# Kernel tuning notes

Measured on AMD Instinct MI355X. Metric: run time of the kernel, lower is better.

Reference implementation:

```python
import jax, jax.numpy as jnp
import numpy as np
import math

NH = 8   # num heads
DH = 64  # d_head = 512/8
D = 512
L = 6

def _pe(seq, d):
    pos = np.arange(seq, dtype=np.float32)[:, None]
    div = np.exp(np.arange(0, d, 2, dtype=np.float32) * (-math.log(10000.0) / d))
    pe = np.zeros((seq, d), dtype=np.float32)
    pe[:, 0::2] = np.sin(pos * div)
    pe[:, 1::2] = np.cos(pos * div)
    return jnp.asarray(pe)

def _ln(x, g, b, eps=1e-6):
    m = x.mean(-1, keepdims=True)
    v = ((x - m) ** 2).mean(-1, keepdims=True)  # unbiased=False
    return g * (x - m) / jnp.sqrt(v + eps) + b

def _mha(q_in, k_in, v_in, qkv_w, qkv_b, o_w, o_b, mask):
    b, sq, d = q_in.shape
    sk = k_in.shape[1]
    q = (q_in @ qkv_w[0] + qkv_b[0]).reshape(b, sq, NH, DH).transpose(0, 2, 1, 3)  # [b,h,sq,dh]
    k = (k_in @ qkv_w[1] + qkv_b[1]).reshape(b, sk, NH, DH).transpose(0, 2, 1, 3)
    v = (v_in @ qkv_w[2] + qkv_b[2]).reshape(b, sk, NH, DH).transpose(0, 2, 1, 3)
    scores = jnp.einsum('bhqd,bhkd->bhqk', q, k) / math.sqrt(DH)  # [b,h,sq,sk]
    if mask is not None:
        scores = jnp.where(mask, -jnp.inf, scores)  # mask True = masked, broadcast over b,h
    w = jax.nn.softmax(scores, axis=-1)
    out = jnp.einsum('bhqk,bhkd->bhqd', w, v).transpose(0, 2, 1, 3).reshape(b, sq, d)
    return out @ o_w + o_b

def _ff(x, w1, b1, w2, b2):
    return jax.nn.relu(x @ w1 + b1) @ w2 + b2

def reference(src, tgt, src_emb, tgt_emb,
              enc_qkv_w, enc_qkv_b, enc_o_w, enc_o_b,
              enc_ff_w1, enc_ff_b1, enc_ff_w2, enc_ff_b2,
              enc_ln_g, enc_ln_b, enc_fg, enc_fb,
              dec_sqkv_w, dec_sqkv_b, dec_so_w, dec_so_b,
              dec_cqkv_w, dec_cqkv_b, dec_co_w, dec_co_b,
              dec_ff_w1, dec_ff_b1, dec_ff_w2, dec_ff_b2,
              dec_ln_g, dec_ln_b, dec_fg, dec_fb):
    S, T = src.shape[1], tgt.shape[1]
    scale = math.sqrt(D)
    # ---- encoder (pre-LN) ----
    x = src_emb[src] * scale + _pe(S, D)  # [b,S,d]
    for i in range(L):
        h = _ln(x, enc_ln_g[i, 0], enc_ln_b[i, 0])
        x = x + _mha(h, h, h, enc_qkv_w[i], enc_qkv_b[i], enc_o_w[i], enc_o_b[i], None)
        h = _ln(x, enc_ln_g[i, 1], enc_ln_b[i, 1])
        x = x + _ff(h, enc_ff_w1[i], enc_ff_b1[i], enc_ff_w2[i], enc_ff_b2[i])
    memory = _ln(x, enc_fg, enc_fb)
    # ---- decoder (pre-LN) ----
    causal = jnp.triu(jnp.ones((T, T), dtype=bool), 1)  # True above diagonal = masked
    y = tgt_emb[tgt] * scale + _pe(T, D)  # [b,T,d]
    for i in range(L):
        h = _ln(y, dec_ln_g[i, 0], dec_ln_b[i, 0])
        y = y + _mha(h, h, h, dec_sqkv_w[i], dec_sqkv_b[i], dec_so_w[i], dec_so_b[i], causal)
        h = _ln(y, dec_ln_g[i, 1], dec_ln_b[i, 1])
        y = y + _mha(h, memory, memory, dec_cqkv_w[i], dec_cqkv_b[i], dec_co_w[i], dec_co_b[i], None)
        h = _ln(y, dec_ln_g[i, 2], dec_ln_b[i, 2])
        y = y + _ff(h, dec_ff_w1[i], dec_ff_b1[i], dec_ff_w2[i], dec_ff_b2[i])
    return _ln(y, dec_fg, dec_fb)

def setup_inputs():
    key = jax.random.key(0)
    ks = iter(jax.random.split(key, 40))
    B, S, T, V, DFF = 8, 128, 128, 32000, 2048
    s = 0.02
    inp = {
        'src': jax.random.randint(next(ks), (B, S), 0, V, dtype=jnp.int32),
        'tgt': jax.random.randint(next(ks), (B, T), 0, V, dtype=jnp.int32),
        'src_emb': jax.random.normal(next(ks), (V, D), jnp.float32) * s,
        'tgt_emb': jax.random.normal(next(ks), (V, D), jnp.float32) * s,
        'enc_qkv_w': jax.random.normal(next(ks), (L, 3, D, D), jnp.float32) * s,
        'enc_qkv_b': jnp.zeros((L, 3, D), jnp.float32),
        'enc_o_w': jax.random.normal(next(ks), (L, D, D), jnp.float32) * s,
        'enc_o_b': jnp.zeros((L, D), jnp.float32),
        'enc_ff_w1': jax.random.normal(next(ks), (L, D, DFF), jnp.float32) * s,
        'enc_ff_b1': jnp.zeros((L, DFF), jnp.float32),
        'enc_ff_w2': jax.random.normal(next(ks), (L, DFF, D), jnp.float32) * s,
        'enc_ff_b2': jnp.zeros((L, D), jnp.float32),
        'enc_ln_g': jnp.ones((L, 2, D), jnp.float32),
        'enc_ln_b': jnp.zeros((L, 2, D), jnp.float32),
        'enc_fg': jnp.ones((D,), jnp.float32),
        'enc_fb': jnp.zeros((D,), jnp.float32),
        'dec_sqkv_w': jax.random.normal(next(ks), (L, 3, D, D), jnp.float32) * s,
        'dec_sqkv_b': jnp.zeros((L, 3, D), jnp.float32),
        'dec_so_w': jax.random.normal(next(ks), (L, D, D), jnp.float32) * s,
        'dec_so_b': jnp.zeros((L, D), jnp.float32),
        'dec_cqkv_w': jax.random.normal(next(ks), (L, 3, D, D), jnp.float32) * s,
        'dec_cqkv_b': jnp.zeros((L, 3, D), jnp.float32),
        'dec_co_w': jax.random.normal(next(ks), (L, D, D), jnp.float32) * s,
        'dec_co_b': jnp.zeros((L, D), jnp.float32),
        'dec_ff_w1': jax.random.normal(next(ks), (L, D, DFF), jnp.float32) * s,
        'dec_ff_b1': jnp.zeros((L, DFF), jnp.float32),
        'dec_ff_w2': jax.random.normal(next(ks), (L, DFF, D), jnp.float32) * s,
        'dec_ff_b2': jnp.zeros((L, D), jnp.float32),
        'dec_ln_g': jnp.ones((L, 3, D), jnp.float32),
        'dec_ln_b': jnp.zeros((L, 3, D), jnp.float32),
        'dec_fg': jnp.ones((D,), jnp.float32),
        'dec_fb': jnp.zeros((D,), jnp.float32),
    }
    return inp
```

## Files before the change

kernel.cpp:

```cpp
#include <hip/hip_runtime.h>
#include <hip/hip_bf16.h>
#include <math.h>

#define D 512
#define NH 8
#define DHEAD 64
#define LAYERS 6
#define DFF 2048
#define BATCH 8
#define SEQ 128
#define ROWS (BATCH * SEQ)

typedef float f32x4 __attribute__((ext_vector_type(4)));
typedef short bf16x8 __attribute__((ext_vector_type(8)));

__device__ __forceinline__ unsigned short f2b(float x) {
    return __builtin_bit_cast(unsigned short, __float2bfloat16(x));
}

__global__ __launch_bounds__(256) void embed_pe_kernel(const int* __restrict__ tok,
        const float* __restrict__ emb, float* __restrict__ out)
{
    int i = blockIdx.x * 256 + threadIdx.x;
    int bs = i >> 9;
    int d  = i & 511;
    int s  = bs & (SEQ - 1);
    int tk = tok[bs];
    float dv  = expf(-(float)(d & ~1) * (9.210340371976184f / 512.0f));
    float arg = (float)s * dv;
    float pe  = (d & 1) ? cosf(arg) : sinf(arg);
    out[i] = emb[(size_t)tk * D + d] * 22.627416997969522f + pe;
}

__global__ __launch_bounds__(256) void transpose_cvt_kernel(
        const float* __restrict__ in, unsigned short* __restrict__ out, int R, int C)
{
    __shared__ float t[32][33];
    const size_t moff = (size_t)blockIdx.z * R * C;
    const float* src = in + moff;
    unsigned short* dst = out + moff;
    const int r0 = blockIdx.y << 5, c0 = blockIdx.x << 5;
    const int tid = threadIdx.x;
    const int rr = tid >> 3, cc = (tid & 7) << 2;
    float4 v = *(const float4*)(src + (size_t)(r0 + rr) * C + c0 + cc);
    t[rr][cc] = v.x; t[rr][cc + 1] = v.y; t[rr][cc + 2] = v.z; t[rr][cc + 3] = v.w;
    __syncthreads();
    const int oc = tid >> 3, or4 = (tid & 7) << 2;
    ushort4 o;
    o.x = f2b(t[or4 + 0][oc]);
    o.y = f2b(t[or4 + 1][oc]);
    o.z = f2b(t[or4 + 2][oc]);
    o.w = f2b(t[or4 + 3][oc]);
    *(ushort4*)(dst + (size_t)(c0 + oc) * R + r0 + or4) = o;
}

template<int OUT_BF16>
__global__ __launch_bounds__(256) void ln_kernel(const float* __restrict__ x,
        const float* __restrict__ g, const float* __restrict__ bta,
        void* __restrict__ outp)
{
    int lane = threadIdx.x & 63;
    int row  = (blockIdx.x << 2) + (threadIdx.x >> 6);
    const float* xr = x + (size_t)row * D;
    int c = lane * 8;
    float4 v0 = *(const float4*)(xr + c);
    float4 v1 = *(const float4*)(xr + c + 4);
    float s  = v0.x + v0.y + v0.z + v0.w + v1.x + v1.y + v1.z + v1.w;
    float sq = v0.x*v0.x + v0.y*v0.y + v0.z*v0.z + v0.w*v0.w
             + v1.x*v1.x + v1.y*v1.y + v1.z*v1.z + v1.w*v1.w;
    #pragma unroll
    for (int o = 32; o; o >>= 1) {
        s  += __shfl_xor(s, o);
        sq += __shfl_xor(sq, o);
    }
    float mean = s * (1.0f / D);
    float var  = sq * (1.0f / D) - mean * mean;
    float inv  = rsqrtf(var + 1e-6f);
    float4 g0 = *(const float4*)(g + c),   g1 = *(const float4*)(g + c + 4);
    float4 b0 = *(const float4*)(bta + c), b1 = *(const float4*)(bta + c + 4);
    float4 o0, o1;
    o0.x = g0.x * (v0.x - mean) * inv + b0.x;
    o0.y = g0.y * (v0.y - mean) * inv + b0.y;
    o0.z = g0.z * (v0.z - mean) * inv + b0.z;
    o0.w = g0.w * (v0.w - mean) * inv + b0.w;
    o1.x = g1.x * (v1.x - mean) * inv + b1.x;
    o1.y = g1.y * (v1.y - mean) * inv + b1.y;
    o1.z = g1.z * (v1.z - mean) * inv + b1.z;
    o1.w = g1.w * (v1.w - mean) * inv + b1.w;
    if (OUT_BF16) {
        unsigned short* orow = (unsigned short*)outp + (size_t)row * D + c;
        uint4 o;
        o.x = (unsigned int)f2b(o0.x) | ((unsigned int)f2b(o0.y) << 16);
        o.y = (unsigned int)f2b(o0.z) | ((unsigned int)f2b(o0.w) << 16);
        o.z = (unsigned int)f2b(o1.x) | ((unsigned int)f2b(o1.y) << 16);
        o.w = (unsigned int)f2b(o1.z) | ((unsigned int)f2b(o1.w) << 16);
        *(uint4*)orow = o;
    } else {
        float* orow = (float*)outp + (size_t)row * D + c;
        *(float4*)(orow)     = o0;
        *(float4*)(orow + 4) = o1;
    }
}

template<int RESID, int RELU, int OUT_BF16>
__global__ __launch_bounds__(256) void mgemm_kernel(
        const unsigned short* __restrict__ A,
        const unsigned short* __restrict__ Wt,
        const float* __restrict__ bias,
        const float* __restrict__ Rp,
        void* __restrict__ Cout,
        int N, int K,
        long aZ, long wZ, long bZ, long cZ)
{
    __shared__ unsigned short As[2][64][72];
    __shared__ unsigned short Bs[2][64][72];
    const long z = blockIdx.z;
    const unsigned short* Ab = A  + z * aZ;
    const unsigned short* Wb = Wt + z * wZ;
    const float* biasb = bias + z * bZ;
    const int tid  = threadIdx.x;
    const int lane = tid & 63, wid = tid >> 6;
    const int wm = wid >> 1, wn = wid & 1;
    const int bm = blockIdx.y << 6, bn = blockIdx.x << 6;
    const int srow = tid >> 2, sk = (tid & 3) << 4;
    const unsigned short* Ag = Ab + (size_t)(bm + srow) * K + sk;
    const unsigned short* Bg = Wb + (size_t)(bn + srow) * K + sk;
    const int fr = lane & 15;
    const int fk = (lane >> 4) << 3;
    f32x4 acc[2][2];
    #pragma unroll
    for (int i = 0; i < 2; ++i)
        #pragma unroll
        for (int j = 0; j < 2; ++j)
            acc[i][j] = (f32x4){0.f, 0.f, 0.f, 0.f};

    uint4 a0 = *(const uint4*)Ag, a1 = *(const uint4*)(Ag + 8);
    uint4 b0 = *(const uint4*)Bg, b1 = *(const uint4*)(Bg + 8);
    const int T = K >> 6;
    for (int t = 0; t < T; ++t) {
        const int p = t & 1;
        *(uint4*)&As[p][srow][sk]     = a0;
        *(uint4*)&As[p][srow][sk + 8] = a1;
        *(uint4*)&Bs[p][srow][sk]     = b0;
        *(uint4*)&Bs[p][srow][sk + 8] = b1;
        if (t + 1 < T) {
            Ag += 64; Bg += 64;
            a0 = *(const uint4*)Ag; a1 = *(const uint4*)(Ag + 8);
            b0 = *(const uint4*)Bg; b1 = *(const uint4*)(Bg + 8);
        }
        __syncthreads();
        #pragma unroll
        for (int s = 0; s < 2; ++s) {
            bf16x8 af0 = *(const bf16x8*)&As[p][wm * 32 + fr][s * 32 + fk];
            bf16x8 af1 = *(const bf16x8*)&As[p][wm * 32 + 16 + fr][s * 32 + fk];
            bf16x8 bf0 = *(const bf16x8*)&Bs[p][wn * 32 + fr][s * 32 + fk];
            bf16x8 bf1 = *(const bf16x8*)&Bs[p][wn * 32 + 16 + fr][s * 32 + fk];
            acc[0][0] = __builtin_amdgcn_mfma_f32_16x16x32_bf16(af0, bf0, acc[0][0], 0, 0, 0);
            acc[0][1] = __builtin_amdgcn_mfma_f32_16x16x32_bf16(af0, bf1, acc[0][1], 0, 0, 0);
            acc[1][0] = __builtin_amdgcn_mfma_f32_16x16x32_bf16(af1, bf0, acc[1][0], 0, 0, 0);
            acc[1][1] = __builtin_amdgcn_mfma_f32_16x16x32_bf16(af1, bf1, acc[1][1], 0, 0, 0);
        }
    }
    const int cr   = (lane >> 4) << 2;
    const int ccol = lane & 15;
    #pragma unroll
    for (int i = 0; i < 2; ++i)
        #pragma unroll
        for (int j = 0; j < 2; ++j) {
            int col = bn + wn * 32 + j * 16 + ccol;
            float bsv = biasb[col];
            #pragma unroll
            for (int r = 0; r < 4; ++r) {
                int row = bm + wm * 32 + i * 16 + cr + r;
                float v = acc[i][j][r] + bsv;
                if (RESID) v += Rp[(size_t)row * N + col];
                if (RELU)  v = fmaxf(v, 0.f);
                if (OUT_BF16) ((unsigned short*)Cout + z * cZ)[(size_t)row * N + col] = f2b(v);
                else          ((float*)Cout)[(size_t)row * N + col] = v;
            }
        }
}

template<int CAUSAL>
__global__ __launch_bounds__(256) void attn_kernel(
        const unsigned short* __restrict__ Qp, int qs,
        const unsigned short* __restrict__ Kp,
        const unsigned short* __restrict__ Vp, int kvs,
        unsigned short* __restrict__ Op, int os)
{
    __shared__ unsigned short Ks[128 * 72];
    __shared__ unsigned short Qs[64 * 72];
    __shared__ unsigned short Vt[64 * 136];
    __shared__ unsigned short Ps[64 * 136];
    const int bh    = blockIdx.x >> 1;
    const int qbase = (blockIdx.x & 1) << 6;
    const int brow  = (bh >> 3) * SEQ;
    const int hoff  = (bh & 7) * DHEAD;
    const int tid = threadIdx.x, lane = tid & 63, wid = tid >> 6;

    #pragma unroll
    for (int it = 0; it < 4; ++it) {
        int idx = it * 256 + tid;
        int row = idx >> 3;
        int c8  = (idx & 7) << 3;
        *(uint4*)&Ks[row * 72 + c8] =
            *(const uint4*)(Kp + (size_t)(brow + row) * kvs + hoff + c8);
        uint4 vu = *(const uint4*)(Vp + (size_t)(brow + row) * kvs + hoff + c8);
        unsigned arr[4] = {vu.x, vu.y, vu.z, vu.w};
        #pragma unroll
        for (int j = 0; j < 8; ++j)
            Vt[(c8 + j) * 136 + row] = (unsigned short)(arr[j >> 1] >> ((j & 1) * 16));
    }
    #pragma unroll
    for (int it = 0; it < 2; ++it) {
        int idx = it * 256 + tid;
        int row = idx >> 3;
        int c8  = (idx & 7) << 3;
        *(uint4*)&Qs[row * 72 + c8] =
            *(const uint4*)(Qp + (size_t)(brow + qbase + row) * qs + hoff + c8);
    }
    __syncthreads();

    const int fr = lane & 15, fg = lane >> 4;
    f32x4 accs[8];
    #pragma unroll
    for (int kf = 0; kf < 8; ++kf) accs[kf] = (f32x4){0.f, 0.f, 0.f, 0.f};
    bf16x8 aq0 = *(const bf16x8*)&Qs[(wid * 16 + fr) * 72 + fg * 8];
    bf16x8 aq1 = *(const bf16x8*)&Qs[(wid * 16 + fr) * 72 + 32 + fg * 8];
    #pragma unroll
    for (int kf = 0; kf < 8; ++kf) {
        bf16x8 bk0 = *(const bf16x8*)&Ks[(kf * 16 + fr) * 72 + fg * 8];
        bf16x8 bk1 = *(const bf16x8*)&Ks[(kf * 16 + fr) * 72 + 32 + fg * 8];
        accs[kf] = __builtin_amdgcn_mfma_f32_16x16x32_bf16(aq0, bk0, accs[kf], 0, 0, 0);
        accs[kf] = __builtin_amdgcn_mfma_f32_16x16x32_bf16(aq1, bk1, accs[kf], 0, 0, 0);
    }
    const float SC = 0.125f * 1.44269504f;
    float linv[4];
    #pragma unroll
    for (int r = 0; r < 4; ++r) {
        int qrow = qbase + wid * 16 + fg * 4 + r;
        float sv[8];
        #pragma unroll
        for (int kf = 0; kf < 8; ++kf) {
            float s = accs[kf][r] * SC;
            if (CAUSAL) {
                int key = kf * 16 + fr;
                if (key > qrow) s = -1e30f;
            }
            sv[kf] = s;
        }
        float m = sv[0];
        #pragma unroll
        for (int kf = 1; kf < 8; ++kf) m = fmaxf(m, sv[kf]);
        #pragma unroll
        for (int o = 1; o < 16; o <<= 1) m = fmaxf(m, __shfl_xor(m, o));
        float l = 0.f;
        #pragma unroll
        for (int kf = 0; kf < 8; ++kf) {
            float p = exp2f(sv[kf] - m);
            l += p;
            Ps[(wid * 16 + fg * 4 + r) * 136 + kf * 16 + fr] = f2b(p);
        }
        #pragma unroll
        for (int o = 1; o < 16; o <<= 1) l += __shfl_xor(l, o);
        linv[r] = 1.f / l;
    }
    f32x4 acco[4];
    #pragma unroll
    for (int df = 0; df < 4; ++df) acco[df] = (f32x4){0.f, 0.f, 0.f, 0.f};
    #pragma unroll
    for (int ks = 0; ks < 4; ++ks) {
        bf16x8 pa = *(const bf16x8*)&Ps[(wid * 16 + fr) * 136 + ks * 32 + fg * 8];
        #pragma unroll
        for (int df = 0; df < 4; ++df) {
            bf16x8 vb = *(const bf16x8*)&Vt[(df * 16 + fr) * 136 + ks * 32 + fg * 8];
            acco[df] = __builtin_amdgcn_mfma_f32_16x16x32_bf16(pa, vb, acco[df], 0, 0, 0);
        }
    }
    #pragma unroll
    for (int df = 0; df < 4; ++df)
        #pragma unroll
        for (int r = 0; r < 4; ++r) {
            int qrow = qbase + wid * 16 + fg * 4 + r;
            Op[(size_t)(brow + qrow) * os + hoff + df * 16 + fr] = f2b(acco[df][r] * linv[r]);
        }
}

extern "C" void kernel_launch(void* const* d_in, const int* in_sizes, int n_in,
                              void* d_out, int out_size, void* d_ws, size_t ws_size,
                              hipStream_t stream)
{
    const int*   src       = (const int*)d_in[0];
    const int*   tgt       = (const int*)d_in[1];
    const float* src_emb   = (const float*)d_in[2];
    const float* tgt_emb   = (const float*)d_in[3];
    const float* enc_qkv_w = (const float*)d_in[4];
    const float* enc_qkv_b = (const float*)d_in[5];
    const float* enc_o_w   = (const float*)d_in[6];
    const float* enc_o_b   = (const float*)d_in[7];
    const float* enc_ff_w1 = (const float*)d_in[8];
    const float* enc_ff_b1 = (const float*)d_in[9];
    const float* enc_ff_w2 = (const float*)d_in[10];
    const float* enc_ff_b2 = (const float*)d_in[11];
    const float* enc_ln_g  = (const float*)d_in[12];
    const float* enc_ln_b  = (const float*)d_in[13];
    const float* enc_fg    = (const float*)d_in[14];
    const float* enc_fb    = (const float*)d_in[15];
    const float* dec_sqkv_w = (const float*)d_in[16];
    const float* dec_sqkv_b = (const float*)d_in[17];
    const float* dec_so_w   = (const float*)d_in[18];
    const float* dec_so_b   = (const float*)d_in[19];
    const float* dec_cqkv_w = (const float*)d_in[20];
    const float* dec_cqkv_b = (const float*)d_in[21];
    const float* dec_co_w   = (const float*)d_in[22];
    const float* dec_co_b   = (const float*)d_in[23];
    const float* dec_ff_w1  = (const float*)d_in[24];
    const float* dec_ff_b1  = (const float*)d_in[25];
    const float* dec_ff_w2  = (const float*)d_in[26];
    const float* dec_ff_b2  = (const float*)d_in[27];
    const float* dec_ln_g   = (const float*)d_in[28];
    const float* dec_ln_b   = (const float*)d_in[29];
    const float* dec_fg     = (const float*)d_in[30];
    const float* dec_fb     = (const float*)d_in[31];

    unsigned short* wp = (unsigned short*)d_ws;
    unsigned short* WencQKV  = wp; wp += (size_t)6 * 786432;
    unsigned short* WencO    = wp; wp += (size_t)6 * 262144;
    unsigned short* WencF1   = wp; wp += (size_t)6 * 1048576;
    unsigned short* WencF2   = wp; wp += (size_t)6 * 1048576;
    unsigned short* WdecSQKV = wp; wp += (size_t)6 * 786432;
    unsigned short* WdecSO   = wp; wp += (size_t)6 * 262144;
    unsigned short* WdecCQKV = wp; wp += (size_t)6 * 786432;
    unsigned short* WdecCO   = wp; wp += (size_t)6 * 262144;
    unsigned short* WdecF1   = wp; wp += (size_t)6 * 1048576;
    unsigned short* WdecF2   = wp; wp += (size_t)6 * 1048576;
    unsigned short* Hb   = wp; wp += ROWS * D;
    unsigned short* QKVb = wp; wp += ROWS * 3 * D;
    unsigned short* CQb  = wp; wp += ROWS * D;
    unsigned short* CKVall = wp; wp += (size_t)6 * ROWS * 1024;
    unsigned short* ATTb = wp; wp += ROWS * D;
    unsigned short* F1b  = wp; wp += ROWS * DFF;
    unsigned short* MEMb = wp; wp += ROWS * D;
    float* X = (float*)wp;

    auto T = [&](const float* in, unsigned short* out, int R_, int C_, int n) {
        transpose_cvt_kernel<<<dim3(C_ / 32, R_ / 32, n), 256, 0, stream>>>(in, out, R_, C_);
    };
    T(enc_qkv_w,  WencQKV,  512, 512, 18);
    T(enc_o_w,    WencO,    512, 512, 6);
    T(enc_ff_w1,  WencF1,   512, DFF, 6);
    T(enc_ff_w2,  WencF2,   DFF, 512, 6);
    T(dec_sqkv_w, WdecSQKV, 512, 512, 18);
    T(dec_so_w,   WdecSO,   512, 512, 6);
    T(dec_cqkv_w, WdecCQKV, 512, 512, 18);
    T(dec_co_w,   WdecCO,   512, 512, 6);
    T(dec_ff_w1,  WdecF1,   512, DFF, 6);
    T(dec_ff_w2,  WdecF2,   DFF, 512, 6);

    embed_pe_kernel<<<2048, 256, 0, stream>>>(src, src_emb, X);
    for (int i = 0; i < LAYERS; ++i) {
        ln_kernel<1><<<256, 256, 0, stream>>>(X, enc_ln_g + (size_t)(i*2+0)*D, enc_ln_b + (size_t)(i*2+0)*D, Hb);
        mgemm_kernel<0,0,1><<<dim3(24,16,1), 256, 0, stream>>>(Hb, WencQKV + (size_t)i*786432,
                enc_qkv_b + (size_t)i*1536, nullptr, QKVb, 1536, 512, 0, 0, 0, 0);
        attn_kernel<0><<<128, 256, 0, stream>>>(QKVb, 1536, QKVb + 512, QKVb + 1024, 1536, ATTb, 512);
        mgemm_kernel<1,0,0><<<dim3(8,16,1), 256, 0, stream>>>(ATTb, WencO + (size_t)i*262144,
                enc_o_b + (size_t)i*512, X, X, 512, 512, 0, 0, 0, 0);
        ln_kernel<1><<<256, 256, 0, stream>>>(X, enc_ln_g + (size_t)(i*2+1)*D, enc_ln_b + (size_t)(i*2+1)*D, Hb);
        mgemm_kernel<0,1,1><<<dim3(32,16,1), 256, 0, stream>>>(Hb, WencF1 + (size_t)i*1048576,
                enc_ff_b1 + (size_t)i*DFF, nullptr, F1b, DFF, 512, 0, 0, 0, 0);
        mgemm_kernel<1,0,0><<<dim3(8,16,1), 256, 0, stream>>>(F1b, WencF2 + (size_t)i*1048576,
                enc_ff_b2 + (size_t)i*512, X, X, 512, DFF, 0, 0, 0, 0);
    }
    ln_kernel<1><<<256, 256, 0, stream>>>(X, enc_fg, enc_fb, MEMb);

    mgemm_kernel<0,0,1><<<dim3(16,16,6), 256, 0, stream>>>(MEMb, WdecCQKV + 262144,
            dec_cqkv_b + 512, nullptr, CKVall, 1024, 512,
            0 , 786432 , 1536 , (long)ROWS * 1024 );

    embed_pe_kernel<<<2048, 256, 0, stream>>>(tgt, tgt_emb, X);
    for (int i = 0; i < LAYERS; ++i) {
        ln_kernel<1><<<256, 256, 0, stream>>>(X, dec_ln_g + (size_t)(i*3+0)*D, dec_ln_b + (size_t)(i*3+0)*D, Hb);
        mgemm_kernel<0,0,1><<<dim3(24,16,1), 256, 0, stream>>>(Hb, WdecSQKV + (size_t)i*786432,
                dec_sqkv_b + (size_t)i*1536, nullptr, QKVb, 1536, 512, 0, 0, 0, 0);
        attn_kernel<1><<<128, 256, 0, stream>>>(QKVb, 1536, QKVb + 512, QKVb + 1024, 1536, ATTb, 512);
        mgemm_kernel<1,0,0><<<dim3(8,16,1), 256, 0, stream>>>(ATTb, WdecSO + (size_t)i*262144,
                dec_so_b + (size_t)i*512, X, X, 512, 512, 0, 0, 0, 0);
        ln_kernel<1><<<256, 256, 0, stream>>>(X, dec_ln_g + (size_t)(i*3+1)*D, dec_ln_b + (size_t)(i*3+1)*D, Hb);
        mgemm_kernel<0,0,1><<<dim3(8,16,1), 256, 0, stream>>>(Hb, WdecCQKV + (size_t)i*786432,
                dec_cqkv_b + (size_t)i*1536, nullptr, CQb, 512, 512, 0, 0, 0, 0);
        {
            const unsigned short* ckv = CKVall + (size_t)i * ROWS * 1024;
            attn_kernel<0><<<128, 256, 0, stream>>>(CQb, 512, ckv, ckv + 512, 1024, ATTb, 512);
        }
        mgemm_kernel<1,0,0><<<dim3(8,16,1), 256, 0, stream>>>(ATTb, WdecCO + (size_t)i*262144,
                dec_co_b + (size_t)i*512, X, X, 512, 512, 0, 0, 0, 0);
        ln_kernel<1><<<256, 256, 0, stream>>>(X, dec_ln_g + (size_t)(i*3+2)*D, dec_ln_b + (size_t)(i*3+2)*D, Hb);
        mgemm_kernel<0,1,1><<<dim3(32,16,1), 256, 0, stream>>>(Hb, WdecF1 + (size_t)i*1048576,
                dec_ff_b1 + (size_t)i*DFF, nullptr, F1b, DFF, 512, 0, 0, 0, 0);
        mgemm_kernel<1,0,0><<<dim3(8,16,1), 256, 0, stream>>>(F1b, WdecF2 + (size_t)i*1048576,
                dec_ff_b2 + (size_t)i*512, X, X, 512, DFF, 0, 0, 0, 0);
    }
    ln_kernel<0><<<256, 256, 0, stream>>>(X, dec_fg, dec_fb, d_out);
}
```

Before: 768.8 us.

## Fuse QKV projection into attention kernels and batch weight transposes

After: 804.8 us. 4.7% more time.

```diff
diff --git a/kernel.cpp b/kernel.cpp
--- a/kernel.cpp
+++ b/kernel.cpp
@@ -32,13 +32,16 @@
     out[i] = emb[(size_t)tk * D + d] * 22.627416997969522f + pe;
 }
 
-__global__ __launch_bounds__(256) void transpose_cvt_kernel(
-        const float* __restrict__ in, unsigned short* __restrict__ out, int R, int C)
+struct TSeg { const float* src; unsigned short* dst; int cnt; };
+struct TMulti { TSeg seg[6]; };
+
+__global__ __launch_bounds__(256) void transpose_multi_kernel(TMulti m, int R, int C)
 {
     __shared__ float t[32][33];
-    const size_t moff = (size_t)blockIdx.z * R * C;
-    const float* src = in + moff;
-    unsigned short* dst = out + moff;
+    int z = blockIdx.z, s = 0;
+    while (z >= m.seg[s].cnt) { z -= m.seg[s].cnt; ++s; }
+    const float* src = m.seg[s].src + (size_t)z * R * C;
+    unsigned short* dst = m.seg[s].dst + (size_t)z * R * C;
     const int r0 = blockIdx.y << 5, c0 = blockIdx.x << 5;
     const int tid = threadIdx.x;
     const int rr = tid >> 3, cc = (tid & 7) << 2;
@@ -182,45 +185,12 @@
 }
 
 template<int CAUSAL>
-__global__ __launch_bounds__(256) void attn_kernel(
-        const unsigned short* __restrict__ Qp, int qs,
-        const unsigned short* __restrict__ Kp,
-        const unsigned short* __restrict__ Vp, int kvs,
-        unsigned short* __restrict__ Op, int os)
-{
-    __shared__ unsigned short Ks[128 * 72];
-    __shared__ unsigned short Qs[64 * 72];
-    __shared__ unsigned short Vt[64 * 136];
-    __shared__ unsigned short Ps[64 * 136];
-    const int bh    = blockIdx.x >> 1;
-    const int qbase = (blockIdx.x & 1) << 6;
-    const int brow  = (bh >> 3) * SEQ;
-    const int hoff  = (bh & 7) * DHEAD;
-    const int tid = threadIdx.x, lane = tid & 63, wid = tid >> 6;
-
-    #pragma unroll
-    for (int it = 0; it < 4; ++it) {
-        int idx = it * 256 + tid;
-        int row = idx >> 3;
-        int c8  = (idx & 7) << 3;
-        *(uint4*)&Ks[row * 72 + c8] =
-            *(const uint4*)(Kp + (size_t)(brow + row) * kvs + hoff + c8);
-        uint4 vu = *(const uint4*)(Vp + (size_t)(brow + row) * kvs + hoff + c8);
-        unsigned arr[4] = {vu.x, vu.y, vu.z, vu.w};
-        #pragma unroll
-        for (int j = 0; j < 8; ++j)
-            Vt[(c8 + j) * 136 + row] = (unsigned short)(arr[j >> 1] >> ((j & 1) * 16));
-    }
-    #pragma unroll
-    for (int it = 0; it < 2; ++it) {
-        int idx = it * 256 + tid;
-        int row = idx >> 3;
-        int c8  = (idx & 7) << 3;
-        *(uint4*)&Qs[row * 72 + c8] =
-            *(const uint4*)(Qp + (size_t)(brow + qbase + row) * qs + hoff + c8);
-    }
-    __syncthreads();
-
+__device__ __forceinline__ void attn_phase(
+        const unsigned short* Ks, const unsigned short* Vt,
+        const unsigned short* Qs, unsigned short* Ps,
+        int qbase, int brow, int hoff, unsigned short* __restrict__ Op,
+        int lane, int wid)
+{
     const int fr = lane & 15, fg = lane >> 4;
     f32x4 accs[8];
     #pragma unroll
@@ -282,8 +252,182 @@
         #pragma unroll
         for (int r = 0; r < 4; ++r) {
             int qrow = qbase + wid * 16 + fg * 4 + r;
-            Op[(size_t)(brow + qrow) * os + hoff + df * 16 + fr] = f2b(acco[df][r] * linv[r]);
-        }
+            Op[(size_t)(brow + qrow) * D + hoff + df * 16 + fr] = f2b(acco[df][r] * linv[r]);
+        }
+}
+
+template<int CAUSAL>
+__global__ __launch_bounds__(256) void fattn_kernel(
+        const unsigned short* __restrict__ Hb,
+        const unsigned short* __restrict__ W,
+        const float* __restrict__ bias,
+        unsigned short* __restrict__ Op)
+{
+    __shared__ __align__(16) char lds[63488];
+    unsigned short* Ks = (unsigned short*)(lds);
+    unsigned short* Vt = (unsigned short*)(lds + 18432);
+    unsigned short* Qs = (unsigned short*)(lds + 35840);
+    unsigned short* Ps = (unsigned short*)(lds + 46080);
+    unsigned short* Hs = (unsigned short*)(lds);
+    unsigned short* Ws = (unsigned short*)(lds + 18432);
+
+    const int bh = blockIdx.x >> 1;
+    const int qbase = (blockIdx.x & 1) << 6;
+    const int h = bh & 7;
+    const int brow = (bh >> 3) * SEQ;
+    const int hoff = h * DHEAD;
+    const int tid = threadIdx.x, lane = tid & 63, wid = tid >> 6;
+    const int fr = lane & 15, fg = lane >> 4;
+
+    f32x4 accK[2][4], accV[2][4], accQ[4];
+    #pragma unroll
+    for (int m = 0; m < 2; ++m)
+        #pragma unroll
+        for (int n = 0; n < 4; ++n) {
+            accK[m][n] = (f32x4){0.f, 0.f, 0.f, 0.f};
+            accV[m][n] = (f32x4){0.f, 0.f, 0.f, 0.f};
+        }
+    #pragma unroll
+    for (int n = 0; n < 4; ++n) accQ[n] = (f32x4){0.f, 0.f, 0.f, 0.f};
+
+    for (int kt = 0; kt < 8; ++kt) {
+        #pragma unroll
+        for (int it = 0; it < 4; ++it) {
+            int idx = it * 256 + tid;
+            int row = idx >> 3, c8 = (idx & 7) << 3;
+            *(uint4*)&Hs[row * 72 + c8] =
+                *(const uint4*)(Hb + (size_t)(brow + row) * 512 + kt * 64 + c8);
+        }
+        #pragma unroll
+        for (int it = 0; it < 6; ++it) {
+            int idx = it * 256 + tid;
+            int w = idx >> 9;
+            int row = (idx >> 3) & 63, c8 = (idx & 7) << 3;
+            *(uint4*)&Ws[w * 4608 + row * 72 + c8] =
+                *(const uint4*)(W + (size_t)(w * 512 + hoff + row) * 512 + kt * 64 + c8);
+        }
+        __syncthreads();
+        #pragma unroll
+        for (int s = 0; s < 2; ++s) {
+            int fk = s * 32 + fg * 8;
+            bf16x8 hm0 = *(const bf16x8*)&Hs[(wid * 32 + fr) * 72 + fk];
+            bf16x8 hm1 = *(const bf16x8*)&Hs[(wid * 32 + 16 + fr) * 72 + fk];
+            bf16x8 hq  = *(const bf16x8*)&Hs[(qbase + wid * 16 + fr) * 72 + fk];
+            #pragma unroll
+            for (int n = 0; n < 4; ++n) {
+                bf16x8 wq = *(const bf16x8*)&Ws[(n * 16 + fr) * 72 + fk];
+                bf16x8 wk = *(const bf16x8*)&Ws[4608 + (n * 16 + fr) * 72 + fk];
+                bf16x8 wv = *(const bf16x8*)&Ws[9216 + (n * 16 + fr) * 72 + fk];
+                accK[0][n] = __builtin_amdgcn_mfma_f32_16x16x32_bf16(hm0, wk, accK[0][n], 0, 0, 0);
+                accK[1][n] = __builtin_amdgcn_mfma_f32_16x16x32_bf16(hm1, wk, accK[1][n], 0, 0, 0);
+                accV[0][n] = __builtin_amdgcn_mfma_f32_16x16x32_bf16(hm0, wv, accV[0][n], 0, 0, 0);
+                accV[1][n] = __builtin_amdgcn_mfma_f32_16x16x32_bf16(hm1, wv, accV[1][n], 0, 0, 0);
+                accQ[n]    = __builtin_amdgcn_mfma_f32_16x16x32_bf16(hq,  wq, accQ[n],    0, 0, 0);
+            }
+        }
+        __syncthreads();
+    }
+    #pragma unroll
+    for (int m = 0; m < 2; ++m)
+        #pragma unroll
+        for (int n = 0; n < 4; ++n) {
+            int d = n * 16 + fr;
+            float bk = bias[512 + hoff + d];
+            float bv = bias[1024 + hoff + d];
+            #pragma unroll
+            for (int r = 0; r < 4; ++r) {
+                int seq = wid * 32 + m * 16 + fg * 4 + r;
+                Ks[seq * 72 + d]  = f2b(accK[m][n][r] + bk);
+                Vt[d * 136 + seq] = f2b(accV[m][n][r] + bv);
+            }
+        }
+    #pragma unroll
+    for (int n = 0; n < 4; ++n) {
+        int d = n * 16 + fr;
+        float bq = bias[hoff + d];
+        #pragma unroll
+        for (int r = 0; r < 4; ++r) {
+            int ql = wid * 16 + fg * 4 + r;
+            Qs[ql * 72 + d] = f2b(accQ[n][r] + bq);
+        }
+    }
+    __syncthreads();
+    attn_phase<CAUSAL>(Ks, Vt, Qs, Ps, qbase, brow, hoff, Op, lane, wid);
+}
+
+__global__ __launch_bounds__(256) void xattn_kernel(
+        const unsigned short* __restrict__ Hb,
+        const unsigned short* __restrict__ Wq,
+        const float* __restrict__ bias,
+        const unsigned short* __restrict__ KV,
+        unsigned short* __restrict__ Op)
+{
+    __shared__ __align__(16) char lds[63488];
+    unsigned short* Ks  = (unsigned short*)(lds);
+    unsigned short* Vt  = (unsigned short*)(lds + 18432);
+    unsigned short* Qs  = (unsigned short*)(lds + 35840);
+    unsigned short* Ps  = (unsigned short*)(lds + 46080);
+    unsigned short* Hs  = (unsigned short*)(lds + 35840);
+    unsigned short* Wqs = (unsigned short*)(lds + 46080);
+
+    const int bh = blockIdx.x >> 1;
+    const int qbase = (blockIdx.x & 1) << 6;
+    const int h = bh & 7;
+    const int brow = (bh >> 3) * SEQ;
+    const int hoff = h * DHEAD;
+    const int tid = threadIdx.x, lane = tid & 63, wid = tid >> 6;
+    const int fr = lane & 15, fg = lane >> 4;
+
+    #pragma unroll
+    for (int it = 0; it < 4; ++it) {
+        int idx = it * 256 + tid;
+        int row = idx >> 3, c8 = (idx & 7) << 3;
+        const unsigned short* kvrow = KV + (size_t)(brow + row) * 1024 + hoff;
+        *(uint4*)&Ks[row * 72 + c8] = *(const uint4*)(kvrow + c8);
+        uint4 vu = *(const uint4*)(kvrow + 512 + c8);
+        unsigned arr[4] = {vu.x, vu.y, vu.z, vu.w};
+        #pragma unroll
+        for (int j = 0; j < 8; ++j)
+            Vt[(c8 + j) * 136 + row] = (unsigned short)(arr[j >> 1] >> ((j & 1) * 16));
+    }
+    f32x4 accQ[4];
+    #pragma unroll
+    for (int n = 0; n < 4; ++n) accQ[n] = (f32x4){0.f, 0.f, 0.f, 0.f};
+    for (int kt = 0; kt < 8; ++kt) {
+        #pragma unroll
+        for (int it = 0; it < 2; ++it) {
+            int idx = it * 256 + tid;
+            int row = idx >> 3, c8 = (idx & 7) << 3;
+            *(uint4*)&Hs[row * 72 + c8] =
+                *(const uint4*)(Hb + (size_t)(brow + qbase + row) * 512 + kt * 64 + c8);
+            *(uint4*)&Wqs[row * 72 + c8] =
+                *(const uint4*)(Wq + (size_t)(hoff + row) * 512 + kt * 64 + c8);
+        }
+        __syncthreads();
+        #pragma unroll
+        for (int s = 0; s < 2; ++s) {
+            int fk = s * 32 + fg * 8;
+            bf16x8 hq = *(const bf16x8*)&Hs[(wid * 16 + fr) * 72 + fk];
+            #pragma unroll
+            for (int n = 0; n < 4; ++n) {
+                bf16x8 wq = *(const bf16x8*)&Wqs[(n * 16 + fr) * 72 + fk];
+                accQ[n] = __builtin_amdgcn_mfma_f32_16x16x32_bf16(hq, wq, accQ[n], 0, 0, 0);
+            }
+        }
+        __syncthreads();
+    }
+    #pragma unroll
+    for (int n = 0; n < 4; ++n) {
+        int d = n * 16 + fr;
+        float bq = bias[hoff + d];
+        #pragma unroll
+        for (int r = 0; r < 4; ++r) {
+            int ql = wid * 16 + fg * 4 + r;
+            Qs[ql * 72 + d] = f2b(accQ[n][r] + bq);
+        }
+    }
+    __syncthreads();
+    attn_phase<0>(Ks, Vt, Qs, Ps, qbase, brow, hoff, Op, lane, wid);
 }
 
 extern "C" void kernel_launch(void* const* d_in, const int* in_sizes, int n_in,
@@ -335,34 +479,37 @@
     unsigned short* WdecF1   = wp; wp += (size_t)6 * 1048576;
     unsigned short* WdecF2   = wp; wp += (size_t)6 * 1048576;
     unsigned short* Hb   = wp; wp += ROWS * D;
-    unsigned short* QKVb = wp; wp += ROWS * 3 * D;
-    unsigned short* CQb  = wp; wp += ROWS * D;
     unsigned short* CKVall = wp; wp += (size_t)6 * ROWS * 1024;
     unsigned short* ATTb = wp; wp += ROWS * D;
     unsigned short* F1b  = wp; wp += ROWS * DFF;
     unsigned short* MEMb = wp; wp += ROWS * D;
     float* X = (float*)wp;
 
-    auto T = [&](const float* in, unsigned short* out, int R_, int C_, int n) {
-        transpose_cvt_kernel<<<dim3(C_ / 32, R_ / 32, n), 256, 0, stream>>>(in, out, R_, C_);
-    };
-    T(enc_qkv_w,  WencQKV,  512, 512, 18);
-    T(enc_o_w,    WencO,    512, 512, 6);
-    T(enc_ff_w1,  WencF1,   512, DFF, 6);
-    T(enc_ff_w2,  WencF2,   DFF, 512, 6);
-    T(dec_sqkv_w, WdecSQKV, 512, 512, 18);
-    T(dec_so_w,   WdecSO,   512, 512, 6);
-    T(dec_cqkv_w, WdecCQKV, 512, 512, 18);
-    T(dec_co_w,   WdecCO,   512, 512, 6);
-    T(dec_ff_w1,  WdecF1,   512, DFF, 6);
-    T(dec_ff_w2,  WdecF2,   DFF, 512, 6);
+    {
+        TMulti mA = {{ {enc_qkv_w,  WencQKV,  18},
+                       {enc_o_w,    WencO,     6},
+                       {dec_sqkv_w, WdecSQKV, 18},
+                       {dec_so_w,   WdecSO,    6},
+                       {dec_cqkv_w, WdecCQKV, 18},
+                       {dec_co_w,   WdecCO,    6} }};
+        transpose_multi_kernel<<<dim3(16, 16, 72), 256, 0, stream>>>(mA, 512, 512);
+        TMulti mB = {{ {enc_ff_w1, WencF1, 6},
+                       {dec_ff_w1, WdecF1, 6},
+                       {nullptr, nullptr, 1 << 30}, {nullptr, nullptr, 1 << 30},
+                       {nullptr, nullptr, 1 << 30}, {nullptr, nullptr, 1 << 30} }};
+        transpose_multi_kernel<<<dim3(64, 16, 12), 256, 0, stream>>>(mB, 512, 2048);
+        TMulti mC = {{ {enc_ff_w2, WencF2, 6},
+                       {dec_ff_w2, WdecF2, 6},
+                       {nullptr, nullptr, 1 << 30}, {nullptr, nullptr, 1 << 30},
+                       {nullptr, nullptr, 1 << 30}, {nullptr, nullptr, 1 << 30} }};
+        transpose_multi_kernel<<<dim3(16, 64, 12), 256, 0, stream>>>(mC, 2048, 512);
+    }
 
     embed_pe_kernel<<<2048, 256, 0, stream>>>(src, src_emb, X);
     for (int i = 0; i < LAYERS; ++i) {
         ln_kernel<1><<<256, 256, 0, stream>>>(X, enc_ln_g + (size_t)(i*2+0)*D, enc_ln_b + (size_t)(i*2+0)*D, Hb);
-        mgemm_kernel<0,0,1><<<dim3(24,16,1), 256, 0, stream>>>(Hb, WencQKV + (size_t)i*786432,
-                enc_qkv_b + (size_t)i*1536, nullptr, QKVb, 1536, 512, 0, 0, 0, 0);
-        attn_kernel<0><<<128, 256, 0, stream>>>(QKVb, 1536, QKVb + 512, QKVb + 1024, 1536, ATTb, 512);
+        fattn_kernel<0><<<128, 256, 0, stream>>>(Hb, WencQKV + (size_t)i*786432,
+                enc_qkv_b + (size_t)i*1536, ATTb);
         mgemm_kernel<1,0,0><<<dim3(8,16,1), 256, 0, stream>>>(ATTb, WencO + (size_t)i*262144,
                 enc_o_b + (size_t)i*512, X, X, 512, 512, 0, 0, 0, 0);
         ln_kernel<1><<<256, 256, 0, stream>>>(X, enc_ln_g + (size_t)(i*2+1)*D, enc_ln_b + (size_t)(i*2+1)*D, Hb);
@@ -375,23 +522,18 @@
 
     mgemm_kernel<0,0,1><<<dim3(16,16,6), 256, 0, stream>>>(MEMb, WdecCQKV + 262144,
             dec_cqkv_b + 512, nullptr, CKVall, 1024, 512,
-            0 , 786432 , 1536 , (long)ROWS * 1024 );
+            0, 786432, 1536, (long)ROWS * 1024);
 
     embed_pe_kernel<<<2048, 256, 0, stream>>>(tgt, tgt_emb, X);
     for (int i = 0; i < LAYERS; ++i) {
         ln_kernel<1><<<256, 256, 0, stream>>>(X, dec_ln_g + (size_t)(i*3+0)*D, dec_ln_b + (size_t)(i*3+0)*D, Hb);
-        mgemm_kernel<0,0,1><<<dim3(24,16,1), 256, 0, stream>>>(Hb, WdecSQKV + (size_t)i*786432,
-                dec_sqkv_b + (size_t)i*1536, nullptr, QKVb, 1536, 512, 0, 0, 0, 0);
-        attn_kernel<1><<<128, 256, 0, stream>>>(QKVb, 1536, QKVb + 512, QKVb + 1024, 1536, ATTb, 512);
+        fattn_kernel<1><<<128, 256, 0, stream>>>(Hb, WdecSQKV + (size_t)i*786432,
+                dec_sqkv_b + (size_t)i*1536, ATTb);
         mgemm_kernel<1,0,0><<<dim3(8,16,1), 256, 0, stream>>>(ATTb, WdecSO + (size_t)i*262144,
                 dec_so_b + (size_t)i*512, X, X, 512, 512, 0, 0, 0, 0);
         ln_kernel<1><<<256, 256, 0, stream>>>(X, dec_ln_g + (size_t)(i*3+1)*D, dec_ln_b + (size_t)(i*3+1)*D, Hb);
-        mgemm_kernel<0,0,1><<<dim3(8,16,1), 256, 0, stream>>>(Hb, WdecCQKV + (size_t)i*786432,
-                dec_cqkv_b + (size_t)i*1536, nullptr, CQb, 512, 512, 0, 0, 0, 0);
-        {
-            const unsigned short* ckv = CKVall + (size_t)i * ROWS * 1024;
-            attn_kernel<0><<<128, 256, 0, stream>>>(CQb, 512, ckv, ckv + 512, 1024, ATTb, 512);
-        }
+        xattn_kernel<<<128, 256, 0, stream>>>(Hb, WdecCQKV + (size_t)i*786432,
+                dec_cqkv_b + (size_t)i*1536, CKVall + (size_t)i*ROWS*1024, ATTb);
         mgemm_kernel<1,0,0><<<dim3(8,16,1), 256, 0, stream>>>(ATTb, WdecCO + (size_t)i*262144,
                 dec_co_b + (size_t)i*512, X, X, 512, 512, 0, 0, 0, 0);
         ln_kernel<1><<<256, 256, 0, stream>>>(X, dec_ln_g + (size_t)(i*3+2)*D, dec_ln_b + (size_t)(i*3+2)*D, Hb);
```
